# Kernel optimization log

Hardware: AMD Instinct MI355X
Metric: run time of the kernel (lower is better)

Reference implementation:

```python
import jax, jax.numpy as jnp
import numpy as np

MARGIN = 40.0


def setup_inputs() -> dict:
    key = jax.random.key(0)
    k1, k2 = jax.random.split(key)
    feat = jax.random.normal(k1, (4096, 512), dtype=jnp.float32)
    targets = jax.random.randint(k2, (4096,), 0, 64, dtype=jnp.int64)
    return {"feat": feat, "targets": targets}


def reference(feat, targets):
    # corr: (n, n) Gram matrix of features
    corr = feat @ feat.T
    # mask[i, j] = True if same class
    mask = targets[:, None] == targets[None, :]
    big = jnp.asarray(jnp.finfo(corr.dtype).max, corr.dtype)
    # per-row min over positives, max over negatives
    corr_ap = jnp.min(jnp.where(mask, corr, big), axis=1)
    corr_an = jnp.max(jnp.where(mask, -big, corr), axis=1)
    # MarginRankingLoss(margin=40) with y = 1: mean(relu(-(ap - an) + margin))
    loss = jnp.mean(jax.nn.relu(corr_an - corr_ap + MARGIN))
    return loss
```

## Files before the change

kernel.cpp:

```cpp
#include <hip/hip_runtime.h>
#include <float.h>
#include <stdint.h>


#define N_ROWS 4096
#define D_K    512
#define BT     128
#define BK     64
#define NTB    (N_ROWS / BT)
#define NTILES (NTB * (NTB + 1) / 2)
#define MARGIN 40.0f
#define FOLD_BLOCKS 16

typedef __bf16 bf16_t;
typedef bf16_t bf16x8 __attribute__((ext_vector_type(8)));
typedef float  floatx4 __attribute__((ext_vector_type(4)));
typedef unsigned short ushort_t;
typedef ushort_t ushortx8 __attribute__((ext_vector_type(8)));

#define GLOAD_LDS16(g, l)                                        \
    __builtin_amdgcn_global_load_lds(                            \
        (const __attribute__((address_space(1))) void*)(g),      \
        (__attribute__((address_space(3))) void*)(l), 16, 0, 0)

__device__ __forceinline__ ushort_t f2bf_rne(float x) {
    uint32_t u = __builtin_bit_cast(uint32_t, x);
    return (ushort_t)((u + 0x7FFFu + ((u >> 16) & 1u)) >> 16);
}

__global__ __launch_bounds__(256) void cast_kernel(
    const float* __restrict__ f, ushort_t* __restrict__ o,
    int* __restrict__ counter)
{
    const int gid = blockIdx.x * 256 + threadIdx.x;
    if (gid == 0) *counter = 0;

    const int i = gid * 8;
    const float4 v0 = *(const float4*)(f + i);
    const float4 v1 = *(const float4*)(f + i + 4);
    ushortx8 r;
    r[0] = f2bf_rne(v0.x); r[1] = f2bf_rne(v0.y);
    r[2] = f2bf_rne(v0.z); r[3] = f2bf_rne(v0.w);
    r[4] = f2bf_rne(v1.x); r[5] = f2bf_rne(v1.y);
    r[6] = f2bf_rne(v1.z); r[7] = f2bf_rne(v1.w);
    *(ushortx8*)(o + i) = r;
}

__global__ __launch_bounds__(512, 6) void gram_mfma_kernel(
    const ushort_t* __restrict__ fb, const int* __restrict__ tgt,
    float* __restrict__ ap_part, float* __restrict__ an_part)
{
    __shared__ __align__(16) ushort_t As[BT * BK];
    __shared__ __align__(16) ushort_t Bs[BT * BK];
    __shared__ int tgI[BT];
    __shared__ int tgJ[BT];

    float* apRed  = (float*)As;
    float* anRed  = apRed  + 4 * BT;
    float* apRedT = anRed  + 4 * BT;
    float* anRedT = apRedT + 2 * BT;

    int bi = 0, rem = blockIdx.x;
    while (rem >= NTB - bi) { rem -= NTB - bi; ++bi; }
    const int bj = bi + rem;

    const int tid  = threadIdx.x;
    const int i0   = bi * BT;
    const int j0   = bj * BT;
    const int lane = tid & 63;
    const int wave = tid >> 6;
    const int wr   = wave >> 2;
    const int wc   = wave & 3;
    const int lr   = lane & 15;
    const int lg   = lane >> 4;
    const int sw   = lr & 7;

    if (tid < BT)            tgI[tid]      = tgt[i0 + tid];
    else if (tid < 2 * BT)   tgJ[tid - BT] = tgt[j0 + tid - BT];

    const int srow = tid >> 3;
    const int schk = (tid & 7) ^ (srow & 7);
    const size_t gA0 = (size_t)(i0 + srow) * D_K + schk * 8;
    const size_t gB0 = (size_t)(j0 + srow) * D_K + schk * 8;
    const size_t gHi = (size_t)64 * D_K;
    char* AsB = (char*)As;
    char* BsB = (char*)Bs;

    floatx4 acc[4][2];
#pragma unroll
    for (int a = 0; a < 4; ++a)
#pragma unroll
        for (int b = 0; b < 2; ++b) acc[a][b] = (floatx4)0.0f;

    for (int k0 = 0; k0 < D_K; k0 += BK) {
        GLOAD_LDS16(fb + gA0 + k0,       AsB + tid * 16);
        GLOAD_LDS16(fb + gA0 + gHi + k0, AsB + 8192 + tid * 16);
        GLOAD_LDS16(fb + gB0 + k0,       BsB + tid * 16);
        GLOAD_LDS16(fb + gB0 + gHi + k0, BsB + 8192 + tid * 16);
        __syncthreads();

#pragma unroll
        for (int h = 0; h < 2; ++h) {
            bf16x8 af[4], bfr[2];
            const int pc = ((h * 4 + lg) ^ sw) * 8;
#pragma unroll
            for (int rg = 0; rg < 4; ++rg)
                af[rg] = *(const bf16x8*)(As + (wr * 64 + rg * 16 + lr) * BK + pc);
#pragma unroll
            for (int cg = 0; cg < 2; ++cg)
                bfr[cg] = *(const bf16x8*)(Bs + (wc * 32 + cg * 16 + lr) * BK + pc);
#pragma unroll
            for (int rg = 0; rg < 4; ++rg)
#pragma unroll
                for (int cg = 0; cg < 2; ++cg)
                    acc[rg][cg] = __builtin_amdgcn_mfma_f32_16x16x32_bf16(
                        af[rg], bfr[cg], acc[rg][cg], 0, 0, 0);
        }
        __syncthreads();
    }

    int tj[2];
#pragma unroll
    for (int cg = 0; cg < 2; ++cg) tj[cg] = tgJ[wc * 32 + cg * 16 + lr];

    float apT[2], anT[2];
#pragma unroll
    for (int cg = 0; cg < 2; ++cg) { apT[cg] = FLT_MAX; anT[cg] = -FLT_MAX; }

#pragma unroll
    for (int rg = 0; rg < 4; ++rg) {
#pragma unroll
        for (int r = 0; r < 4; ++r) {
            const int rloc = wr * 64 + rg * 16 + lg * 4 + r;
            const int ti = tgI[rloc];
            float vap = FLT_MAX, van = -FLT_MAX;
#pragma unroll
            for (int cg = 0; cg < 2; ++cg) {
                const float v = acc[rg][cg][r];
                if (ti == tj[cg]) { vap = fminf(vap, v); apT[cg] = fminf(apT[cg], v); }
                else              { van = fmaxf(van, v); anT[cg] = fmaxf(anT[cg], v); }
            }
#pragma unroll
            for (int m = 1; m < 16; m <<= 1) {
                vap = fminf(vap, __shfl_xor(vap, m));
                van = fmaxf(van, __shfl_xor(van, m));
            }
            if (lr == 0) { apRed[wc * BT + rloc] = vap; anRed[wc * BT + rloc] = van; }
        }
    }
#pragma unroll
    for (int cg = 0; cg < 2; ++cg) {
        float vap = apT[cg], van = anT[cg];
        vap = fminf(vap, __shfl_xor(vap, 16)); van = fmaxf(van, __shfl_xor(van, 16));
        vap = fminf(vap, __shfl_xor(vap, 32)); van = fmaxf(van, __shfl_xor(van, 32));
        if (lg == 0) {
            apRedT[wr * BT + wc * 32 + cg * 16 + lr] = vap;
            anRedT[wr * BT + wc * 32 + cg * 16 + lr] = van;
        }
    }
    __syncthreads();

    if (tid < BT) {
        const float ap = fminf(fminf(apRed[0 * BT + tid], apRed[1 * BT + tid]),
                               fminf(apRed[2 * BT + tid], apRed[3 * BT + tid]));
        const float an = fmaxf(fmaxf(anRed[0 * BT + tid], anRed[1 * BT + tid]),
                               fmaxf(anRed[2 * BT + tid], anRed[3 * BT + tid]));
        ap_part[(size_t)bj * N_ROWS + i0 + tid] = ap;
        an_part[(size_t)bj * N_ROWS + i0 + tid] = an;
        if (bi != bj) {
            ap_part[(size_t)bi * N_ROWS + j0 + tid] =
                fminf(apRedT[0 * BT + tid], apRedT[1 * BT + tid]);
            an_part[(size_t)bi * N_ROWS + j0 + tid] =
                fmaxf(anRedT[0 * BT + tid], anRedT[1 * BT + tid]);
        }
    }
}

__global__ __launch_bounds__(256) void fold_kernel(
    const float* __restrict__ ap_part, const float* __restrict__ an_part,
    float* __restrict__ blk_sum, int* __restrict__ counter,
    float* __restrict__ out)
{
    __shared__ float sred[4];
    const int tid = threadIdx.x;
    const int row = blockIdx.x * 256 + tid;
    const int lane = tid & 63;
    const int wave = tid >> 6;

    float ap = FLT_MAX, an = -FLT_MAX;
#pragma unroll 8
    for (int s = 0; s < NTB; ++s) {
        ap = fminf(ap, ap_part[(size_t)s * N_ROWS + row]);
        an = fmaxf(an, an_part[(size_t)s * N_ROWS + row]);
    }
    const float v = an - ap + MARGIN;
    float local = (v > 0.0f) ? v : 0.0f;
#pragma unroll
    for (int m = 32; m >= 1; m >>= 1) local += __shfl_down(local, m);
    if (lane == 0) sred[wave] = local;
    __syncthreads();

    if (tid == 0) {
        blk_sum[blockIdx.x] = sred[0] + sred[1] + sred[2] + sred[3];
        __threadfence();
        if (atomicAdd(counter, 1) == FOLD_BLOCKS - 1) {
            __threadfence();
            float s = 0.0f;
#pragma unroll
            for (int b = 0; b < FOLD_BLOCKS; ++b) s += blk_sum[b];
            out[0] = s * (1.0f / N_ROWS);
        }
    }
}

extern "C" void kernel_launch(void* const* d_in, const int* in_sizes, int n_in,
                              void* d_out, int out_size, void* d_ws, size_t ws_size,
                              hipStream_t stream)
{
    const float* feat = (const float*)d_in[0];
    const int*   tgt  = (const int*)d_in[1];

    ushort_t* fb      = (ushort_t*)d_ws;
    float*    ap_part = (float*)(fb + (size_t)N_ROWS * D_K);
    float*    an_part = ap_part + (size_t)NTB * N_ROWS;
    float*    blk_sum = an_part + (size_t)NTB * N_ROWS;
    int*      counter = (int*)(blk_sum + FOLD_BLOCKS);

    cast_kernel<<<(N_ROWS * D_K) / (256 * 8), 256, 0, stream>>>(feat, fb, counter);
    gram_mfma_kernel<<<NTILES, 512, 0, stream>>>(fb, tgt, ap_part, an_part);
    fold_kernel<<<FOLD_BLOCKS, 256, 0, stream>>>(ap_part, an_part, blk_sum,
                                                 counter, (float*)d_out);
}
```

Before: 86.55 us.

## Fuse fold reduction into gram kernel using ticket-based last-blocks finalization

Removes the separate fold kernel launch. Each gram tile block takes a ticket after writing its partials, and the last 32 blocks to finish spin-wait until all tiles are done. They then each reduce a strip of rows, and a second ticket counter picks the final block that sums the strip results into the loss. This saves a kernel launch and its gap, but adds spin-waiting and lower parallelism for the fold, since it runs in 32 blocks using 128 threads each.

```diff
diff --git a/kernel.cpp b/kernel.cpp
--- a/kernel.cpp
+++ b/kernel.cpp
@@ -10,7 +10,8 @@
 #define NTB    (N_ROWS / BT)
 #define NTILES (NTB * (NTB + 1) / 2)
 #define MARGIN 40.0f
-#define FOLD_BLOCKS 16
+#define NSTRIP 32
+#define SROWS  (N_ROWS / NSTRIP)
 
 typedef __bf16 bf16_t;
 typedef bf16_t bf16x8 __attribute__((ext_vector_type(8)));
@@ -30,10 +31,10 @@
 
 __global__ __launch_bounds__(256) void cast_kernel(
     const float* __restrict__ f, ushort_t* __restrict__ o,
-    int* __restrict__ counter)
+    int* __restrict__ tickets)
 {
     const int gid = blockIdx.x * 256 + threadIdx.x;
-    if (gid == 0) *counter = 0;
+    if (gid < 2) tickets[gid] = 0;
 
     const int i = gid * 8;
     const float4 v0 = *(const float4*)(f + i);
@@ -48,12 +49,15 @@
 
 __global__ __launch_bounds__(512, 6) void gram_mfma_kernel(
     const ushort_t* __restrict__ fb, const int* __restrict__ tgt,
-    float* __restrict__ ap_part, float* __restrict__ an_part)
+    float* __restrict__ ap_part, float* __restrict__ an_part,
+    float* __restrict__ blk_sum, int* __restrict__ tickets,
+    float* __restrict__ out)
 {
     __shared__ __align__(16) ushort_t As[BT * BK];
     __shared__ __align__(16) ushort_t Bs[BT * BK];
     __shared__ int tgI[BT];
     __shared__ int tgJ[BT];
+    __shared__ int ticket_s;
 
     float* apRed  = (float*)As;
     float* anRed  = apRed  + 4 * BT;
@@ -174,41 +178,47 @@
                 fmaxf(anRedT[0 * BT + tid], anRedT[1 * BT + tid]);
         }
     }
-}
-
-__global__ __launch_bounds__(256) void fold_kernel(
-    const float* __restrict__ ap_part, const float* __restrict__ an_part,
-    float* __restrict__ blk_sum, int* __restrict__ counter,
-    float* __restrict__ out)
-{
-    __shared__ float sred[4];
-    const int tid = threadIdx.x;
-    const int row = blockIdx.x * 256 + tid;
-    const int lane = tid & 63;
-    const int wave = tid >> 6;
-
-    float ap = FLT_MAX, an = -FLT_MAX;
+
+    __syncthreads();
+    if (tid == 0) {
+        __threadfence();
+        ticket_s = atomicAdd(&tickets[0], 1);
+    }
+    __syncthreads();
+    const int ticket = ticket_s;
+    if (ticket < NTILES - NSTRIP) return;
+    const int strip = ticket - (NTILES - NSTRIP);
+
+    if (tid == 0) {
+        while (__hip_atomic_load(&tickets[0], __ATOMIC_RELAXED,
+                                 __HIP_MEMORY_SCOPE_AGENT) < NTILES)
+            __builtin_amdgcn_s_sleep(2);
+        __threadfence();
+    }
+    __syncthreads();
+
+    if (tid < SROWS) {
+        const int row = strip * SROWS + tid;
+        float ap = FLT_MAX, an = -FLT_MAX;
 #pragma unroll 8
-    for (int s = 0; s < NTB; ++s) {
-        ap = fminf(ap, ap_part[(size_t)s * N_ROWS + row]);
-        an = fmaxf(an, an_part[(size_t)s * N_ROWS + row]);
-    }
-    const float v = an - ap + MARGIN;
-    float local = (v > 0.0f) ? v : 0.0f;
-#pragma unroll
-    for (int m = 32; m >= 1; m >>= 1) local += __shfl_down(local, m);
-    if (lane == 0) sred[wave] = local;
-    __syncthreads();
-
-    if (tid == 0) {
-        blk_sum[blockIdx.x] = sred[0] + sred[1] + sred[2] + sred[3];
-        __threadfence();
-        if (atomicAdd(counter, 1) == FOLD_BLOCKS - 1) {
+        for (int s = 0; s < NTB; ++s) {
+            ap = fminf(ap, ap_part[(size_t)s * N_ROWS + row]);
+            an = fmaxf(an, an_part[(size_t)s * N_ROWS + row]);
+        }
+        const float v = an - ap + MARGIN;
+        float local = (v > 0.0f) ? v : 0.0f;
+#pragma unroll
+        for (int m = 32; m >= 1; m >>= 1) local += __shfl_down(local, m);
+        if (lane == 0) {
+            blk_sum[strip * 2 + wave] = local;
             __threadfence();
-            float s = 0.0f;
-#pragma unroll
-            for (int b = 0; b < FOLD_BLOCKS; ++b) s += blk_sum[b];
-            out[0] = s * (1.0f / N_ROWS);
+            if (atomicAdd(&tickets[1], 1) == 2 * NSTRIP - 1) {
+                __threadfence();
+                float s = 0.0f;
+#pragma unroll 8
+                for (int b = 0; b < 2 * NSTRIP; ++b) s += blk_sum[b];
+                out[0] = s * (1.0f / N_ROWS);
+            }
         }
     }
 }
@@ -224,10 +234,9 @@
     float*    ap_part = (float*)(fb + (size_t)N_ROWS * D_K);
     float*    an_part = ap_part + (size_t)NTB * N_ROWS;
     float*    blk_sum = an_part + (size_t)NTB * N_ROWS;
-    int*      counter = (int*)(blk_sum + FOLD_BLOCKS);
-
-    cast_kernel<<<(N_ROWS * D_K) / (256 * 8), 256, 0, stream>>>(feat, fb, counter);
-    gram_mfma_kernel<<<NTILES, 512, 0, stream>>>(fb, tgt, ap_part, an_part);
-    fold_kernel<<<FOLD_BLOCKS, 256, 0, stream>>>(ap_part, an_part, blk_sum,
-                                                 counter, (float*)d_out);
-}
+    int*      tickets = (int*)(blk_sum + 2 * NSTRIP);
+
+    cast_kernel<<<(N_ROWS * D_K) / (256 * 8), 256, 0, stream>>>(feat, fb, tickets);
+    gram_mfma_kernel<<<NTILES, 512, 0, stream>>>(fb, tgt, ap_part, an_part,
+                                                 blk_sum, tickets, (float*)d_out);
+}
```

Result: slower. 96.46 us (+11.4%).
